# Optimization experiments

Hardware: AMD Instinct MI355X
Metric: run time of the kernel (lower is better)

Reference implementation:

```python
import jax, jax.numpy as jnp
import numpy as np

B, N, C = 512, 32, 1024


def setup_inputs() -> dict:
    key = jax.random.key(0)
    k1, k2, k3 = jax.random.split(key, 3)
    x = jax.random.normal(k1, (B, N, C), dtype=jnp.float32)
    # Conv1d(in=2, out=1, kernel_size=3): weight [O, I, W], bias [O]
    fan_in = 2 * 3
    bound = 1.0 / np.sqrt(fan_in)
    conv_w = jax.random.uniform(k2, (1, 2, 3), dtype=jnp.float32, minval=-bound, maxval=bound)
    conv_b = jax.random.uniform(k3, (1,), dtype=jnp.float32, minval=-bound, maxval=bound)
    return {"x": x, "conv_w": conv_w, "conv_b": conv_b}


def _merge_step(x, conv_w, conv_b):
    # x: [B, n, C] -> [B, n-1, C]
    b, n, c = x.shape
    # pairwise euclidean distances via gram matrix (avoids [B,n,n,C] blowup)
    sq = jnp.sum(x * x, axis=-1)  # [B, n]
    d2 = sq[:, :, None] + sq[:, None, :] - 2.0 * jnp.einsum('bic,bjc->bij', x, x)
    dist = jnp.sqrt(jnp.maximum(d2, 0.0))  # [B, n, n]
    # global max over ALL batches (as torch.max(all_dist)), then mask diagonal
    m = jnp.max(dist)
    di = jnp.arange(n)
    dist = dist.at[:, di, di].set(m + 1.0)
    # per-batch argmin over flattened matrix, unravel
    flat_idx = jnp.argmin(dist.reshape(b, -1), axis=1)
    a = flat_idx // n
    bb = flat_idx % n
    a, bb = jnp.minimum(a, bb), jnp.maximum(a, bb)  # ensure a < b
    # replicate the exact (buggy-faithful) index-list construction:
    # rows[a]=0; rows[0]=a; rows[b]=1; rows[1]=b  (sequential assignments)
    bi = jnp.arange(b)
    perm = jnp.broadcast_to(jnp.arange(n), (b, n))
    perm = perm.at[bi, a].set(0)
    perm = perm.at[bi, 0].set(a)
    perm = perm.at[bi, bb].set(1)
    perm = perm.at[bi, 1].set(bb)
    xg = jnp.take_along_axis(x, perm[:, :, None], axis=1)  # [B, n, C]
    to_merge = xg[:, 0:2, :]      # [B, 2, C]
    remaining = xg[:, 2:, :]      # [B, n-2, C]
    merged = jax.lax.conv_general_dilated(
        to_merge, conv_w, window_strides=(1,), padding='SAME',
        dimension_numbers=('NCH', 'OIH', 'NCH'))  # [B, 1, C]
    merged = jax.nn.relu(merged + conv_b[None, :, None])
    return jnp.concatenate([merged, remaining], axis=1)


def reference(x, conv_w, conv_b):
    b, n, c = x.shape
    for _ in range(n - 1):
        x = _merge_step(x, conv_w, conv_b)
    return x[:, 0, :]  # final squeeze: [B, C]
```

## Files before the change

### kernel.cpp

```cpp
#include <hip/hip_runtime.h>
#include <stdint.h>

#define BDIM    512
#define NROWS   32
#define CDIM    1024
#define NSTEPS  31
#define BATCH   512

__device__ __forceinline__ float reduce4f(float a0, float a1, float a2, float a3, int lane) {
    float t, r, b01, b23, c;
    t = (lane & 1) ? a0 : a1; r = (lane & 1) ? a1 : a0; b01 = r + __shfl_xor(t, 1);
    t = (lane & 1) ? a2 : a3; r = (lane & 1) ? a3 : a2; b23 = r + __shfl_xor(t, 1);
    t = (lane & 2) ? b01 : b23; r = (lane & 2) ? b23 : b01; c = r + __shfl_xor(t, 2);
    c += __shfl_xor(c, 4); c += __shfl_xor(c, 8); c += __shfl_xor(c, 16); c += __shfl_xor(c, 32);
    return c;
}

__global__ __launch_bounds__(BDIM, 4)
void merge_tree_kernel(const float* __restrict__ xin,
                       const float* __restrict__ wz,
                       const float* __restrict__ bz,
                       float* __restrict__ out)
{
    const int b    = blockIdx.x;
    const int tid  = threadIdx.x;
    const int lane = tid & 63;
    const int wid  = tid >> 6;

    const float* xb = xin + (size_t)b * NROWS * CDIM;

    __shared__ float  D[NROWS][NROWS + 1];
    __shared__ float4 mA4[4 * 64];
    __shared__ float4 mB4[4 * 64];
    __shared__ int    idxbuf[2][NROWS];
    __shared__ int    pairTab[496];
    __shared__ unsigned long long wp[8];

    const float w00 = wz[0], w01 = wz[1], w02 = wz[2];
    const float w10 = wz[3], w11 = wz[4], w12 = wz[5];
    const float cb  = bz[0];

    float R[4][16];
    float m[16];
    float nxt[16];
    int   bs[4];
    #pragma unroll
    for (int k = 0; k < 4; k++) bs[k] = wid + (k << 3);

    if (tid < NROWS) {
        idxbuf[0][tid] = tid;
        int i = tid;
        int base = 31 * i - (i * (i - 1)) / 2;
        for (int j = i + 1; j < NROWS; j++)
            pairTab[base + (j - i - 1)] = (i << 8) | j;
    }

    {
        const float4* src = (const float4*)xb;
        #pragma unroll
        for (int q = 0; q < 4; q++) {
            float4 t = src[lane * 4 + q];
            m[4*q] = t.x; m[4*q+1] = t.y; m[4*q+2] = t.z; m[4*q+3] = t.w;
        }
    }
    #pragma unroll 1
    for (int i = 0; i < NROWS; i++) {
        if (i < NROWS - 1) {
            const float4* src = (const float4*)(xb + (size_t)(i + 1) * CDIM);
            #pragma unroll
            for (int q = 0; q < 4; q++) {
                float4 t = src[lane * 4 + q];
                nxt[4*q] = t.x; nxt[4*q+1] = t.y; nxt[4*q+2] = t.z; nxt[4*q+3] = t.w;
            }
        }
        float accv[4];
        #pragma unroll
        for (int k = 0; k < 4; k++) {
            const int s = wid + (k << 3);
            float acc0 = 0.0f, acc1 = 0.0f;
            if (s < i) {
                #pragma unroll
                for (int e = 0; e < 8; e++) {
                    float d0 = m[e] - R[k][e];
                    float d1 = m[e + 8] - R[k][e + 8];
                    acc0 += d0 * d0;
                    acc1 += d1 * d1;
                }
            } else if (s == i) {
                #pragma unroll
                for (int e = 0; e < 16; e++) R[k][e] = m[e];
            }
            accv[k] = acc0 + acc1;
        }
        float c = reduce4f(accv[0], accv[1], accv[2], accv[3], lane);
        int s_lane = wid + ((lane & 3) << 3);
        if (lane < 4 && s_lane < i) { D[i][s_lane] = c; D[s_lane][i] = c; }

        if (i < NROWS - 1) {
            #pragma unroll
            for (int e = 0; e < 16; e++) m[e] = nxt[e];
        }
    }
    __syncthreads();

    int p = 0;
    #pragma unroll 1
    for (int step = 0; step < NSTEPS; step++) {
        const int n = NROWS - step;
        int* idx  = idxbuf[p];
        int* nidx = idxbuf[p ^ 1];
        const uint32_t M = 0xFFFFFFFFu / (uint32_t)n + 1u;

        unsigned long long bk = ~0ull;
        if (tid < 496) {
            const int pr = pairTab[tid];
            const int i2 = pr >> 8, j2 = pr & 255;
            if (j2 < n) {
                const int si = idx[i2], sj = idx[j2];
                uint32_t d2b = __float_as_uint(D[si][sj]);
                bk = ((unsigned long long)d2b << 10) | (unsigned)(i2 * n + j2);
            }
        }
        #pragma unroll
        for (int off = 1; off < 64; off <<= 1) {
            unsigned long long ov = __shfl_xor(bk, off);
            bk = (ov < bk) ? ov : bk;
        }
        if (lane == 0) wp[wid] = bk;
        __syncthreads();

        bk = wp[0];
        #pragma unroll
        for (int w = 1; w < 8; w++) {
            unsigned long long ov = wp[w];
            bk = (ov < bk) ? ov : bk;
        }
        const int bp  = (int)(bk & 1023u);
        const int a   = (int)__umulhi((uint32_t)bp, M);
        const int bbj = bp - a * n;
        const int sa  = idx[a], sb = idx[bbj];
        const int deadSlot = (a == 1) ? idx[0] : sa;

        #pragma unroll
        for (int k = 0; k < 4; k++) {
            const int s = bs[k];
            if (s == sa || s == sb) {
                float hl = __shfl_up(R[k][15], 1);  if (lane == 0)  hl = 0.0f;
                float hr = __shfl_down(R[k][0], 1); if (lane == 63) hr = 0.0f;
                float4* dst = (s == sa) ? mA4 : mB4;
                const float c0 = (s == sa) ? w00 : w10;
                const float c1 = (s == sa) ? w01 : w11;
                const float c2 = (s == sa) ? w02 : w12;
                #pragma unroll
                for (int q = 0; q < 4; q++) {
                    float vv[4];
                    #pragma unroll
                    for (int j = 0; j < 4; j++) {
                        const int e = 4 * q + j;
                        float xm1 = (e == 0)  ? hl : R[k][e - 1];
                        float xp1 = (e == 15) ? hr : R[k][e + 1];
                        vv[j] = c0 * xm1 + c1 * R[k][e] + c2 * xp1;
                    }
                    dst[q * 64 + lane] = make_float4(vv[0], vv[1], vv[2], vv[3]);
                }
            }
        }
        if (tid == 0) nidx[0] = sb;
        if (tid >= 1 && tid < n - 1) {
            int kk = tid + 1;
            int src = (kk == bbj) ? 1 : ((kk == a) ? 0 : kk);
            nidx[tid] = idx[src];
        }
        __syncthreads();

        #pragma unroll
        for (int q = 0; q < 4; q++) {
            float4 va = mA4[q * 64 + lane];
            float4 vb = mB4[q * 64 + lane];
            float v0 = cb + va.x + vb.x;
            float v1 = cb + va.y + vb.y;
            float v2 = cb + va.z + vb.z;
            float v3 = cb + va.w + vb.w;
            m[4*q+0] = v0 > 0.0f ? v0 : 0.0f;
            m[4*q+1] = v1 > 0.0f ? v1 : 0.0f;
            m[4*q+2] = v2 > 0.0f ? v2 : 0.0f;
            m[4*q+3] = v3 > 0.0f ? v3 : 0.0f;
        }
        float accv[4]; int slv[4];
        #pragma unroll
        for (int k = 0; k < 4; k++) {
            int s = bs[k];
            if (s == sb) {
                #pragma unroll
                for (int e = 0; e < 16; e++) R[k][e] = m[e];
            }
            if (s == deadSlot) {
                bs[k] = -1;
                s = -1;
            }
            const int live = (s >= 0 && s != sb) ? s : -1;
            slv[k] = live;
            float acc0 = 0.0f, acc1 = 0.0f;
            if (live >= 0) {
                #pragma unroll
                for (int e = 0; e < 8; e++) {
                    float d0 = m[e] - R[k][e];
                    float d1 = m[e + 8] - R[k][e + 8];
                    acc0 += d0 * d0;
                    acc1 += d1 * d1;
                }
            }
            accv[k] = acc0 + acc1;
        }
        float c = reduce4f(accv[0], accv[1], accv[2], accv[3], lane);
        int s_lane = slv[0];
        s_lane = ((lane & 3) == 1) ? slv[1] : s_lane;
        s_lane = ((lane & 3) == 2) ? slv[2] : s_lane;
        s_lane = ((lane & 3) == 3) ? slv[3] : s_lane;
        if (lane < 4 && s_lane >= 0) {
            D[sb][s_lane] = c; D[s_lane][sb] = c;
        }
        __syncthreads();
        p ^= 1;
    }

    if (wid == 0) {
        float4* od = (float4*)(out + (size_t)b * CDIM);
        #pragma unroll
        for (int q = 0; q < 4; q++)
            od[lane * 4 + q] = make_float4(m[4*q], m[4*q+1], m[4*q+2], m[4*q+3]);
    }
}

extern "C" void kernel_launch(void* const* d_in, const int* in_sizes, int n_in,
                              void* d_out, int out_size, void* d_ws, size_t ws_size,
                              hipStream_t stream) {
    const float* x  = (const float*)d_in[0];
    const float* w  = (const float*)d_in[1];
    const float* cb = (const float*)d_in[2];
    float* out = (float*)d_out;
    (void)d_ws; (void)ws_size; (void)in_sizes; (void)n_in; (void)out_size;

    hipLaunchKernelGGL(merge_tree_kernel, dim3(BATCH), dim3(BDIM), 0, stream,
                       x, w, cb, out);
}
```

Before: 204.1 us.

## Process two batches per block to halve barrier count per batch

Each block now handles two batch elements, interleaving their merge steps so every __syncthreads and argmin reduction round covers both. Register state doubles (R, m, bs per batch), and launch bounds drop to 2 blocks per SM. The goal is to amortize barrier and latency overhead and give more ILP, at the cost of register pressure, lower occupancy and only 256 blocks for the GPU.

```diff
diff --git a/kernel.cpp b/kernel.cpp
--- a/kernel.cpp
+++ b/kernel.cpp
@@ -16,89 +16,94 @@
     return c;
 }
 
-__global__ __launch_bounds__(BDIM, 4)
+__global__ __launch_bounds__(BDIM, 2)
 void merge_tree_kernel(const float* __restrict__ xin,
                        const float* __restrict__ wz,
                        const float* __restrict__ bz,
                        float* __restrict__ out)
 {
-    const int b    = blockIdx.x;
+    const int b0   = blockIdx.x * 2;
     const int tid  = threadIdx.x;
     const int lane = tid & 63;
     const int wid  = tid >> 6;
 
-    const float* xb = xin + (size_t)b * NROWS * CDIM;
-
-    __shared__ float  D[NROWS][NROWS + 1];
-    __shared__ float4 mA4[4 * 64];
-    __shared__ float4 mB4[4 * 64];
-    __shared__ int    idxbuf[2][NROWS];
+    __shared__ float  D[2][NROWS][NROWS + 1];
+    __shared__ float4 mA4[2][4 * 64];
+    __shared__ float4 mB4[2][4 * 64];
+    __shared__ int    idxbuf[2][2][NROWS];
     __shared__ int    pairTab[496];
-    __shared__ unsigned long long wp[8];
+    __shared__ unsigned long long wp[2][8];
 
     const float w00 = wz[0], w01 = wz[1], w02 = wz[2];
     const float w10 = wz[3], w11 = wz[4], w12 = wz[5];
     const float cb  = bz[0];
 
-    float R[4][16];
-    float m[16];
-    float nxt[16];
-    int   bs[4];
+    float R[2][4][16];
+    float m[2][16];
+    int   bs[2][4];
     #pragma unroll
-    for (int k = 0; k < 4; k++) bs[k] = wid + (k << 3);
+    for (int h = 0; h < 2; h++)
+        #pragma unroll
+        for (int k = 0; k < 4; k++) bs[h][k] = wid + (k << 3);
 
     if (tid < NROWS) {
-        idxbuf[0][tid] = tid;
+        idxbuf[0][0][tid] = tid;
+        idxbuf[1][0][tid] = tid;
         int i = tid;
         int base = 31 * i - (i * (i - 1)) / 2;
         for (int j = i + 1; j < NROWS; j++)
             pairTab[base + (j - i - 1)] = (i << 8) | j;
     }
 
-    {
-        const float4* src = (const float4*)xb;
-        #pragma unroll
-        for (int q = 0; q < 4; q++) {
-            float4 t = src[lane * 4 + q];
-            m[4*q] = t.x; m[4*q+1] = t.y; m[4*q+2] = t.z; m[4*q+3] = t.w;
-        }
-    }
-    #pragma unroll 1
-    for (int i = 0; i < NROWS; i++) {
-        if (i < NROWS - 1) {
-            const float4* src = (const float4*)(xb + (size_t)(i + 1) * CDIM);
+    #pragma unroll
+    for (int h = 0; h < 2; h++) {
+        const float* xb = xin + (size_t)(b0 + h) * NROWS * CDIM;
+        float mm[16], nxt[16];
+        {
+            const float4* src = (const float4*)xb;
             #pragma unroll
             for (int q = 0; q < 4; q++) {
                 float4 t = src[lane * 4 + q];
-                nxt[4*q] = t.x; nxt[4*q+1] = t.y; nxt[4*q+2] = t.z; nxt[4*q+3] = t.w;
-            }
-        }
-        float accv[4];
-        #pragma unroll
-        for (int k = 0; k < 4; k++) {
-            const int s = wid + (k << 3);
-            float acc0 = 0.0f, acc1 = 0.0f;
-            if (s < i) {
+                mm[4*q] = t.x; mm[4*q+1] = t.y; mm[4*q+2] = t.z; mm[4*q+3] = t.w;
+            }
+        }
+        #pragma unroll 1
+        for (int i = 0; i < NROWS; i++) {
+            if (i < NROWS - 1) {
+                const float4* src = (const float4*)(xb + (size_t)(i + 1) * CDIM);
                 #pragma unroll
-                for (int e = 0; e < 8; e++) {
-                    float d0 = m[e] - R[k][e];
-                    float d1 = m[e + 8] - R[k][e + 8];
-                    acc0 += d0 * d0;
-                    acc1 += d1 * d1;
-                }
-            } else if (s == i) {
+                for (int q = 0; q < 4; q++) {
+                    float4 t = src[lane * 4 + q];
+                    nxt[4*q] = t.x; nxt[4*q+1] = t.y; nxt[4*q+2] = t.z; nxt[4*q+3] = t.w;
+                }
+            }
+            float accv[4];
+            #pragma unroll
+            for (int k = 0; k < 4; k++) {
+                const int s = wid + (k << 3);
+                float acc0 = 0.0f, acc1 = 0.0f;
+                if (s < i) {
+                    #pragma unroll
+                    for (int e = 0; e < 8; e++) {
+                        float d0 = mm[e] - R[h][k][e];
+                        float d1 = mm[e + 8] - R[h][k][e + 8];
+                        acc0 += d0 * d0;
+                        acc1 += d1 * d1;
+                    }
+                } else if (s == i) {
+                    #pragma unroll
+                    for (int e = 0; e < 16; e++) R[h][k][e] = mm[e];
+                }
+                accv[k] = acc0 + acc1;
+            }
+            float c = reduce4f(accv[0], accv[1], accv[2], accv[3], lane);
+            int s_lane = wid + ((lane & 3) << 3);
+            if (lane < 4 && s_lane < i) { D[h][i][s_lane] = c; D[h][s_lane][i] = c; }
+
+            if (i < NROWS - 1) {
                 #pragma unroll
-                for (int e = 0; e < 16; e++) R[k][e] = m[e];
-            }
-            accv[k] = acc0 + acc1;
-        }
-        float c = reduce4f(accv[0], accv[1], accv[2], accv[3], lane);
-        int s_lane = wid + ((lane & 3) << 3);
-        if (lane < 4 && s_lane < i) { D[i][s_lane] = c; D[s_lane][i] = c; }
-
-        if (i < NROWS - 1) {
-            #pragma unroll
-            for (int e = 0; e < 16; e++) m[e] = nxt[e];
+                for (int e = 0; e < 16; e++) mm[e] = nxt[e];
+            }
         }
     }
     __syncthreads();
@@ -107,128 +112,145 @@
     #pragma unroll 1
     for (int step = 0; step < NSTEPS; step++) {
         const int n = NROWS - step;
-        int* idx  = idxbuf[p];
-        int* nidx = idxbuf[p ^ 1];
         const uint32_t M = 0xFFFFFFFFu / (uint32_t)n + 1u;
 
-        unsigned long long bk = ~0ull;
+        unsigned long long bk0 = ~0ull, bk1 = ~0ull;
         if (tid < 496) {
             const int pr = pairTab[tid];
             const int i2 = pr >> 8, j2 = pr & 255;
             if (j2 < n) {
-                const int si = idx[i2], sj = idx[j2];
-                uint32_t d2b = __float_as_uint(D[si][sj]);
-                bk = ((unsigned long long)d2b << 10) | (unsigned)(i2 * n + j2);
+                const int si0 = idxbuf[0][p][i2], sj0 = idxbuf[0][p][j2];
+                const int si1 = idxbuf[1][p][i2], sj1 = idxbuf[1][p][j2];
+                const unsigned fl = (unsigned)(i2 * n + j2);
+                uint32_t d0 = __float_as_uint(D[0][si0][sj0]);
+                uint32_t d1 = __float_as_uint(D[1][si1][sj1]);
+                bk0 = ((unsigned long long)d0 << 10) | fl;
+                bk1 = ((unsigned long long)d1 << 10) | fl;
             }
         }
         #pragma unroll
         for (int off = 1; off < 64; off <<= 1) {
-            unsigned long long ov = __shfl_xor(bk, off);
-            bk = (ov < bk) ? ov : bk;
-        }
-        if (lane == 0) wp[wid] = bk;
+            unsigned long long o0 = __shfl_xor(bk0, off);
+            unsigned long long o1 = __shfl_xor(bk1, off);
+            bk0 = (o0 < bk0) ? o0 : bk0;
+            bk1 = (o1 < bk1) ? o1 : bk1;
+        }
+        if (lane == 0) { wp[0][wid] = bk0; wp[1][wid] = bk1; }
         __syncthreads();
 
-        bk = wp[0];
-        #pragma unroll
-        for (int w = 1; w < 8; w++) {
-            unsigned long long ov = wp[w];
-            bk = (ov < bk) ? ov : bk;
-        }
-        const int bp  = (int)(bk & 1023u);
-        const int a   = (int)__umulhi((uint32_t)bp, M);
-        const int bbj = bp - a * n;
-        const int sa  = idx[a], sb = idx[bbj];
-        const int deadSlot = (a == 1) ? idx[0] : sa;
-
-        #pragma unroll
-        for (int k = 0; k < 4; k++) {
-            const int s = bs[k];
-            if (s == sa || s == sb) {
-                float hl = __shfl_up(R[k][15], 1);  if (lane == 0)  hl = 0.0f;
-                float hr = __shfl_down(R[k][0], 1); if (lane == 63) hr = 0.0f;
-                float4* dst = (s == sa) ? mA4 : mB4;
-                const float c0 = (s == sa) ? w00 : w10;
-                const float c1 = (s == sa) ? w01 : w11;
-                const float c2 = (s == sa) ? w02 : w12;
-                #pragma unroll
-                for (int q = 0; q < 4; q++) {
-                    float vv[4];
-                    #pragma unroll
-                    for (int j = 0; j < 4; j++) {
-                        const int e = 4 * q + j;
-                        float xm1 = (e == 0)  ? hl : R[k][e - 1];
-                        float xp1 = (e == 15) ? hr : R[k][e + 1];
-                        vv[j] = c0 * xm1 + c1 * R[k][e] + c2 * xp1;
+        int a_[2], bbj_[2], sa_[2], sb_[2], dead_[2];
+        #pragma unroll
+        for (int h = 0; h < 2; h++) {
+            unsigned long long bk = wp[h][0];
+            #pragma unroll
+            for (int w = 1; w < 8; w++) {
+                unsigned long long ov = wp[h][w];
+                bk = (ov < bk) ? ov : bk;
+            }
+            const int bp = (int)(bk & 1023u);
+            a_[h]   = (int)__umulhi((uint32_t)bp, M);
+            bbj_[h] = bp - a_[h] * n;
+            sa_[h]  = idxbuf[h][p][a_[h]];
+            sb_[h]  = idxbuf[h][p][bbj_[h]];
+            dead_[h] = (a_[h] == 1) ? idxbuf[h][p][0] : sa_[h];
+        }
+        #pragma unroll
+        for (int h = 0; h < 2; h++) {
+            #pragma unroll
+            for (int k = 0; k < 4; k++) {
+                const int s = bs[h][k];
+                if (s == sa_[h] || s == sb_[h]) {
+                    float hl = __shfl_up(R[h][k][15], 1);  if (lane == 0)  hl = 0.0f;
+                    float hr = __shfl_down(R[h][k][0], 1); if (lane == 63) hr = 0.0f;
+                    float4* dst = (s == sa_[h]) ? mA4[h] : mB4[h];
+                    const float c0 = (s == sa_[h]) ? w00 : w10;
+                    const float c1 = (s == sa_[h]) ? w01 : w11;
+                    const float c2 = (s == sa_[h]) ? w02 : w12;
+                    #pragma unroll
+                    for (int q = 0; q < 4; q++) {
+                        float vv[4];
+                        #pragma unroll
+                        for (int j = 0; j < 4; j++) {
+                            const int e = 4 * q + j;
+                            float xm1 = (e == 0)  ? hl : R[h][k][e - 1];
+                            float xp1 = (e == 15) ? hr : R[h][k][e + 1];
+                            vv[j] = c0 * xm1 + c1 * R[h][k][e] + c2 * xp1;
+                        }
+                        dst[q * 64 + lane] = make_float4(vv[0], vv[1], vv[2], vv[3]);
                     }
-                    dst[q * 64 + lane] = make_float4(vv[0], vv[1], vv[2], vv[3]);
-                }
-            }
-        }
-        if (tid == 0) nidx[0] = sb;
-        if (tid >= 1 && tid < n - 1) {
-            int kk = tid + 1;
-            int src = (kk == bbj) ? 1 : ((kk == a) ? 0 : kk);
-            nidx[tid] = idx[src];
+                }
+            }
+            if (tid == 0) idxbuf[h][p ^ 1][0] = sb_[h];
+            if (tid >= 1 && tid < n - 1) {
+                int kk = tid + 1;
+                int src = (kk == bbj_[h]) ? 1 : ((kk == a_[h]) ? 0 : kk);
+                idxbuf[h][p ^ 1][tid] = idxbuf[h][p][src];
+            }
         }
         __syncthreads();
 
         #pragma unroll
-        for (int q = 0; q < 4; q++) {
-            float4 va = mA4[q * 64 + lane];
-            float4 vb = mB4[q * 64 + lane];
-            float v0 = cb + va.x + vb.x;
-            float v1 = cb + va.y + vb.y;
-            float v2 = cb + va.z + vb.z;
-            float v3 = cb + va.w + vb.w;
-            m[4*q+0] = v0 > 0.0f ? v0 : 0.0f;
-            m[4*q+1] = v1 > 0.0f ? v1 : 0.0f;
-            m[4*q+2] = v2 > 0.0f ? v2 : 0.0f;
-            m[4*q+3] = v3 > 0.0f ? v3 : 0.0f;
-        }
-        float accv[4]; int slv[4];
-        #pragma unroll
-        for (int k = 0; k < 4; k++) {
-            int s = bs[k];
-            if (s == sb) {
-                #pragma unroll
-                for (int e = 0; e < 16; e++) R[k][e] = m[e];
-            }
-            if (s == deadSlot) {
-                bs[k] = -1;
-                s = -1;
-            }
-            const int live = (s >= 0 && s != sb) ? s : -1;
-            slv[k] = live;
-            float acc0 = 0.0f, acc1 = 0.0f;
-            if (live >= 0) {
-                #pragma unroll
-                for (int e = 0; e < 8; e++) {
-                    float d0 = m[e] - R[k][e];
-                    float d1 = m[e + 8] - R[k][e + 8];
-                    acc0 += d0 * d0;
-                    acc1 += d1 * d1;
-                }
-            }
-            accv[k] = acc0 + acc1;
-        }
-        float c = reduce4f(accv[0], accv[1], accv[2], accv[3], lane);
-        int s_lane = slv[0];
-        s_lane = ((lane & 3) == 1) ? slv[1] : s_lane;
-        s_lane = ((lane & 3) == 2) ? slv[2] : s_lane;
-        s_lane = ((lane & 3) == 3) ? slv[3] : s_lane;
-        if (lane < 4 && s_lane >= 0) {
-            D[sb][s_lane] = c; D[s_lane][sb] = c;
+        for (int h = 0; h < 2; h++) {
+            #pragma unroll
+            for (int q = 0; q < 4; q++) {
+                float4 va = mA4[h][q * 64 + lane];
+                float4 vb = mB4[h][q * 64 + lane];
+                float v0 = cb + va.x + vb.x;
+                float v1 = cb + va.y + vb.y;
+                float v2 = cb + va.z + vb.z;
+                float v3 = cb + va.w + vb.w;
+                m[h][4*q+0] = v0 > 0.0f ? v0 : 0.0f;
+                m[h][4*q+1] = v1 > 0.0f ? v1 : 0.0f;
+                m[h][4*q+2] = v2 > 0.0f ? v2 : 0.0f;
+                m[h][4*q+3] = v3 > 0.0f ? v3 : 0.0f;
+            }
+            float accv[4]; int slv[4];
+            #pragma unroll
+            for (int k = 0; k < 4; k++) {
+                int s = bs[h][k];
+                if (s == sb_[h]) {
+                    #pragma unroll
+                    for (int e = 0; e < 16; e++) R[h][k][e] = m[h][e];
+                }
+                if (s == dead_[h]) {
+                    bs[h][k] = -1;
+                    s = -1;
+                }
+                const int live = (s >= 0 && s != sb_[h]) ? s : -1;
+                slv[k] = live;
+                float acc0 = 0.0f, acc1 = 0.0f;
+                if (live >= 0) {
+                    #pragma unroll
+                    for (int e = 0; e < 8; e++) {
+                        float d0 = m[h][e] - R[h][k][e];
+                        float d1 = m[h][e + 8] - R[h][k][e + 8];
+                        acc0 += d0 * d0;
+                        acc1 += d1 * d1;
+                    }
+                }
+                accv[k] = acc0 + acc1;
+            }
+            float c = reduce4f(accv[0], accv[1], accv[2], accv[3], lane);
+            int s_lane = slv[0];
+            s_lane = ((lane & 3) == 1) ? slv[1] : s_lane;
+            s_lane = ((lane & 3) == 2) ? slv[2] : s_lane;
+            s_lane = ((lane & 3) == 3) ? slv[3] : s_lane;
+            if (lane < 4 && s_lane >= 0) {
+                D[h][sb_[h]][s_lane] = c; D[h][s_lane][sb_[h]] = c;
+            }
         }
         __syncthreads();
         p ^= 1;
     }
 
-    if (wid == 0) {
-        float4* od = (float4*)(out + (size_t)b * CDIM);
-        #pragma unroll
-        for (int q = 0; q < 4; q++)
-            od[lane * 4 + q] = make_float4(m[4*q], m[4*q+1], m[4*q+2], m[4*q+3]);
+    #pragma unroll
+    for (int h = 0; h < 2; h++) {
+        if (wid == h) {
+            float4* od = (float4*)(out + (size_t)(b0 + h) * CDIM);
+            #pragma unroll
+            for (int q = 0; q < 4; q++)
+                od[lane * 4 + q] = make_float4(m[h][4*q], m[h][4*q+1], m[h][4*q+2], m[h][4*q+3]);
+        }
     }
 }
 
@@ -241,6 +263,6 @@
     float* out = (float*)d_out;
     (void)d_ws; (void)ws_size; (void)in_sizes; (void)n_in; (void)out_size;
 
-    hipLaunchKernelGGL(merge_tree_kernel, dim3(BATCH), dim3(BDIM), 0, stream,
+    hipLaunchKernelGGL(merge_tree_kernel, dim3(BATCH / 2), dim3(BDIM), 0, stream,
                        x, w, cb, out);
 }
```

After: 275.8 us. 1.35x slower.

## Fold row-0 pair minimum into previous step to drop a barrier per merge

Applied to the files above, without the earlier changes.

Distance updates for the newly merged row (position 0) are now reduced into a per-wave candidate key at the end of each step. Each wave writes its key into an extra slot of the shared partials, and an npos table maps slots to positions so the keys carry the right pair index. The pair table now covers only pairs with both positions at least 1 (465 entries), and the final cross-wave minimum reads 16 partials. This removes the trailing __syncthreads from every step, in exchange for extra shared bookkeeping and reliance on the remaining barriers to keep the D, npos and wp accesses ordered.

```diff
diff --git a/kernel.cpp b/kernel.cpp
--- a/kernel.cpp
+++ b/kernel.cpp
@@ -33,8 +33,9 @@
     __shared__ float4 mA4[4 * 64];
     __shared__ float4 mB4[4 * 64];
     __shared__ int    idxbuf[2][NROWS];
-    __shared__ int    pairTab[496];
-    __shared__ unsigned long long wp[8];
+    __shared__ int    npos[NROWS];
+    __shared__ int    pairTab[465];
+    __shared__ unsigned long long wp[16];
 
     const float w00 = wz[0], w01 = wz[1], w02 = wz[2];
     const float w10 = wz[3], w11 = wz[4], w12 = wz[5];
@@ -50,10 +51,13 @@
     if (tid < NROWS) {
         idxbuf[0][tid] = tid;
         int i = tid;
-        int base = 31 * i - (i * (i - 1)) / 2;
-        for (int j = i + 1; j < NROWS; j++)
-            pairTab[base + (j - i - 1)] = (i << 8) | j;
-    }
+        if (i >= 1 && i < 31) {
+            int base = 31 * (i - 1) - (i * (i - 1)) / 2;
+            for (int j = i + 1; j < NROWS; j++)
+                pairTab[base + (j - i - 1)] = (i << 8) | j;
+        }
+    }
+    if (tid < 16) wp[tid] = ~0ull;
 
     {
         const float4* src = (const float4*)xb;
@@ -103,6 +107,20 @@
     }
     __syncthreads();
 
+    if (wid == 0) {
+        unsigned long long sk = ~0ull;
+        if (lane < 31) {
+            uint32_t d2b = __float_as_uint(D[0][lane + 1]);
+            sk = ((unsigned long long)d2b << 10) | (unsigned)(lane + 1);
+        }
+        #pragma unroll
+        for (int off = 1; off < 64; off <<= 1) {
+            unsigned long long ov = __shfl_xor(sk, off);
+            sk = (ov < sk) ? ov : sk;
+        }
+        if (lane == 0) wp[8] = sk;
+    }
+
     int p = 0;
     #pragma unroll 1
     for (int step = 0; step < NSTEPS; step++) {
@@ -112,7 +130,7 @@
         const uint32_t M = 0xFFFFFFFFu / (uint32_t)n + 1u;
 
         unsigned long long bk = ~0ull;
-        if (tid < 496) {
+        if (tid < 465) {
             const int pr = pairTab[tid];
             const int i2 = pr >> 8, j2 = pr & 255;
             if (j2 < n) {
@@ -131,7 +149,7 @@
 
         bk = wp[0];
         #pragma unroll
-        for (int w = 1; w < 8; w++) {
+        for (int w = 1; w < 16; w++) {
             unsigned long long ov = wp[w];
             bk = (ov < bk) ? ov : bk;
         }
@@ -165,11 +183,13 @@
                 }
             }
         }
-        if (tid == 0) nidx[0] = sb;
+        if (tid == 0) { nidx[0] = sb; npos[sb] = 0; }
         if (tid >= 1 && tid < n - 1) {
             int kk = tid + 1;
             int src = (kk == bbj) ? 1 : ((kk == a) ? 0 : kk);
-            nidx[tid] = idx[src];
+            int sl2 = idx[src];
+            nidx[tid] = sl2;
+            npos[sl2] = tid;
         }
         __syncthreads();
 
@@ -217,10 +237,17 @@
         s_lane = ((lane & 3) == 1) ? slv[1] : s_lane;
         s_lane = ((lane & 3) == 2) ? slv[2] : s_lane;
         s_lane = ((lane & 3) == 3) ? slv[3] : s_lane;
+        unsigned long long nk = ~0ull;
         if (lane < 4 && s_lane >= 0) {
             D[sb][s_lane] = c; D[s_lane][sb] = c;
-        }
-        __syncthreads();
+            const int fl = npos[s_lane];
+            nk = ((unsigned long long)__float_as_uint(c) << 10) | (unsigned)fl;
+        }
+        {
+            unsigned long long ov = __shfl_xor(nk, 1); nk = (ov < nk) ? ov : nk;
+            ov = __shfl_xor(nk, 2);                    nk = (ov < nk) ? ov : nk;
+        }
+        if (lane == 0) wp[8 + wid] = nk;
         p ^= 1;
     }
 
```

Result: slower. 216.2 us (+6.0%).
